# Optimization experiments

Hardware: AMD Instinct MI355X
Metric: run time of the kernel (lower is better)

## Reference

```python
import jax, jax.numpy as jnp
import numpy as np

B, L, D, M = 4, 8192, 512, 256
EPS = 1e-6


def _feature_map(x, proj, is_query):
    # FAVOR+ positive softmax-kernel features.
    # x: (B, L, D), proj: (M, D) with orthogonal rows scaled by sqrt(D).
    d = x.shape[-1]
    xs = x * (d ** -0.25)                      # scale by d^{-1/4}
    dash = jnp.einsum('bld,md->blm', xs, proj)  # (B, L, M)
    diag = 0.5 * jnp.sum(xs * xs, axis=-1, keepdims=True)  # (B, L, 1)
    if is_query:
        stab = jnp.max(dash, axis=-1, keepdims=True)        # per-position max
    else:
        stab = jnp.max(dash, axis=(-2, -1), keepdims=True)  # per-batch max
    return jnp.exp(dash - diag - stab) / jnp.sqrt(jnp.asarray(M, x.dtype)) + EPS


def setup_inputs() -> dict:
    key = jax.random.key(0)
    kq, kk, kv, kp = jax.random.split(key, 4)
    Q = jax.random.normal(kq, (B, L, D), dtype=jnp.float32)
    K = jax.random.normal(kk, (B, L, D), dtype=jnp.float32)
    V = jax.random.normal(kv, (B, L, D), dtype=jnp.float32)
    # Orthogonal random projection: QR of a Gaussian, rows scaled by sqrt(D).
    G = jax.random.normal(kp, (D, M), dtype=jnp.float32)
    q, _ = jnp.linalg.qr(G)                     # (D, M), orthonormal columns
    proj = q.T * jnp.sqrt(jnp.asarray(D, jnp.float32))  # (M, D)
    return {"Q": Q, "K": K, "V": V, "proj": proj}


def reference(Q, K, V, proj):
    Qf = _feature_map(Q, proj, is_query=True)   # (B, L, M)
    Kf = _feature_map(K, proj, is_query=False)  # (B, L, M)
    # Linear attention: aggregate keys/values once, O(L*M*D).
    KV = jnp.einsum('blm,bld->bmd', Kf, V)      # (B, M, D)
    Ksum = jnp.sum(Kf, axis=1)                  # (B, M)
    Z = 1.0 / (jnp.einsum('blm,bm->bl', Qf, Ksum) + EPS)  # (B, L)
    out = jnp.einsum('blm,bmd->bld', Qf, KV) * Z[..., None]
    return out
```

## Files before the change

kernel.cpp:

```cpp
#include <hip/hip_runtime.h>
#include <math.h>

typedef unsigned short u16;
typedef unsigned int u32;
typedef __attribute__((ext_vector_type(8))) short bf16x8;
typedef __attribute__((ext_vector_type(4))) float f32x4;

#define SCALE_ 0.21022410381342864f
#define EPS_ 1e-6f
#define RSQM_ 0.0625f
#define L_ 8192
#define PL_OFF_ 131072
#define KVL_OFF_ 524288

__device__ __forceinline__ float bf2f(u16 h) {
    return __uint_as_float(((u32)h) << 16);
}
__device__ __forceinline__ u32 cvtpk(float x0, float x1) {
    u32 w;
    asm("v_cvt_pk_bf16_f32 %0, %1, %2" : "=v"(w) : "v"(x0), "v"(x1));
    return w;
}
__device__ __forceinline__ void split_pk(float x0, float x1, u32& hw, u32& lw) {
    hw = cvtpk(x0, x1);
    float h0 = __uint_as_float(hw << 16);
    float h1 = __uint_as_float(hw & 0xffff0000u);
    lw = cvtpk(x0 - h0, x1 - h1);
}
__device__ __forceinline__ u32 okey(float x) {
    u32 b = __float_as_uint(x);
    return (b & 0x80000000u) ? ~b : (b | 0x80000000u);
}
__device__ __forceinline__ float odec(u32 k) {
    return (k & 0x80000000u) ? __uint_as_float(k & 0x7fffffffu) : __uint_as_float(~k);
}

#define GLDS16(gsrc, ldst) \
    __builtin_amdgcn_global_load_lds((__attribute__((address_space(1))) void*)(gsrc), \
                                     (__attribute__((address_space(3))) void*)(ldst), 16, 0, 0)

__global__ __launch_bounds__(256) void split_p(const float* __restrict__ P,
        u16* __restrict__ Ph, u16* __restrict__ Pl, u32* __restrict__ bmax) {
    if (blockIdx.x == 0 && threadIdx.x < 4) bmax[threadIdx.x] = 0u;
    int i = (blockIdx.x * 256 + threadIdx.x) * 2;
    u32 hw, lw;
    split_pk(P[i] * SCALE_, P[i + 1] * SCALE_, hw, lw);
    *reinterpret_cast<u32*>(&Ph[i]) = hw;
    *reinterpret_cast<u32*>(&Pl[i]) = lw;
}

__global__ __launch_bounds__(256) void dash_all(
        const float* __restrict__ Qg, const float* __restrict__ Kg,
        const u16* __restrict__ Bh_g,
        u16* __restrict__ QF, u16* __restrict__ KfT, float* __restrict__ ksump,
        u32* __restrict__ bmax) {
    __shared__ __align__(16) u16 Ah[64 * 32], Al[64 * 32];
    __shared__ __align__(16) u16 Bh[256 * 32], Bl[256 * 32];
    const int qpath = !(blockIdx.x & 1);
    const int tile = blockIdx.x >> 1;
    const float* __restrict__ X = qpath ? Qg : Kg;
    const int t = threadIdx.x, lane = t & 63;
    const int wid = t >> 6;
    const int row0 = tile * 64;
    const int l15 = lane & 15, l4 = lane >> 4;
    const int sr = t >> 2;
    const int awz = sr * 32 + (((t & 3) ^ ((sr >> 1) & 3)) * 8);
    const int koff = (l4 ^ ((l15 >> 1) & 3)) * 8;
    float ss = 0.f;

    const float* xp = &X[(size_t)(row0 + sr) * 512 + (t & 3) * 8];
    const u16* bsrch[4];
#pragma unroll
    for (int it = 0; it < 4; ++it) {
        const int m = it * 64 + wid * 16 + (lane >> 2);
        const int swz = ((lane & 3) ^ ((m >> 1) & 3)) * 8;
        bsrch[it] = Bh_g + (size_t)m * 512 + swz;
    }

    f32x4 acc[4][4];
#pragma unroll
    for (int i = 0; i < 4; ++i)
#pragma unroll
        for (int j = 0; j < 4; ++j) acc[i][j] = (f32x4){0.f, 0.f, 0.f, 0.f};

    float4 v0 = *reinterpret_cast<const float4*>(xp);
    float4 v1 = *reinterpret_cast<const float4*>(xp + 4);

    for (int kt = 0; kt < 16; ++kt) {
        __syncthreads();
        {
#pragma unroll
            for (int it = 0; it < 4; ++it) {
                GLDS16(bsrch[it], Bh + it * 2048 + wid * 512);
                GLDS16(bsrch[it] + PL_OFF_, Bl + it * 2048 + wid * 512);
                bsrch[it] += 32;
            }
            float xs[8] = {v0.x, v0.y, v0.z, v0.w, v1.x, v1.y, v1.z, v1.w};
#pragma unroll
            for (int i = 0; i < 8; ++i) ss = fmaf(xs[i], xs[i], ss);
            u32 hw[4], lw[4];
#pragma unroll
            for (int i = 0; i < 4; ++i) split_pk(xs[2 * i], xs[2 * i + 1], hw[i], lw[i]);
            *reinterpret_cast<uint4*>(&Ah[awz]) = make_uint4(hw[0], hw[1], hw[2], hw[3]);
            *reinterpret_cast<uint4*>(&Al[awz]) = make_uint4(lw[0], lw[1], lw[2], lw[3]);
            xp = (kt < 15) ? xp + 32 : xp;
            v0 = *reinterpret_cast<const float4*>(xp);
            v1 = *reinterpret_cast<const float4*>(xp + 4);
        }
        __syncthreads();
        bf16x8 a_h[4], a_l[4];
#pragma unroll
        for (int mf = 0; mf < 4; ++mf) {
            int r = (mf * 16 + l15) * 32 + koff;
            a_h[mf] = *reinterpret_cast<const bf16x8*>(&Ah[r]);
            a_l[mf] = *reinterpret_cast<const bf16x8*>(&Al[r]);
        }
#pragma unroll
        for (int nf = 0; nf < 4; ++nf) {
            const int r = (wid * 64 + nf * 16 + l15) * 32 + koff;
            bf16x8 b_h = *reinterpret_cast<const bf16x8*>(&Bh[r]);
            bf16x8 b_l = *reinterpret_cast<const bf16x8*>(&Bl[r]);
#pragma unroll
            for (int mf = 0; mf < 4; ++mf) {
                acc[mf][nf] = __builtin_amdgcn_mfma_f32_16x16x32_bf16(a_h[mf], b_h, acc[mf][nf], 0, 0, 0);
                acc[mf][nf] = __builtin_amdgcn_mfma_f32_16x16x32_bf16(a_h[mf], b_l, acc[mf][nf], 0, 0, 0);
                acc[mf][nf] = __builtin_amdgcn_mfma_f32_16x16x32_bf16(a_l[mf], b_h, acc[mf][nf], 0, 0, 0);
            }
        }
    }
    __syncthreads();
    float* rmaxp = reinterpret_cast<float*>(Ah);
    float* diagp = reinterpret_cast<float*>(Al);

    ss += __shfl_xor(ss, 1);
    ss += __shfl_xor(ss, 2);
    if ((t & 3) == 0) diagp[sr] = 0.5f * SCALE_ * SCALE_ * ss;

    if (qpath) {
        float rm[4][4];
#pragma unroll
        for (int mf = 0; mf < 4; ++mf)
#pragma unroll
            for (int r = 0; r < 4; ++r) {
                float v = fmaxf(fmaxf(acc[mf][0][r], acc[mf][1][r]),
                                fmaxf(acc[mf][2][r], acc[mf][3][r]));
#pragma unroll
                for (int off = 1; off < 16; off <<= 1) v = fmaxf(v, __shfl_xor(v, off));
                rm[mf][r] = v;
            }
        if (l15 == 0) {
#pragma unroll
            for (int mf = 0; mf < 4; ++mf)
#pragma unroll
                for (int r = 0; r < 4; ++r)
                    rmaxp[(mf * 16 + l4 * 4 + r) * 4 + wid] = rm[mf][r];
        }
        __syncthreads();
#pragma unroll
        for (int mf = 0; mf < 4; ++mf)
#pragma unroll
            for (int r = 0; r < 4; ++r) {
                const int rl = mf * 16 + l4 * 4 + r;
                float m4 = fmaxf(fmaxf(rmaxp[rl * 4 + 0], rmaxp[rl * 4 + 1]),
                                 fmaxf(rmaxp[rl * 4 + 2], rmaxp[rl * 4 + 3]));
                const float c = diagp[rl] + m4;
                float f0 = expf(acc[mf][0][r] - c) * RSQM_ + EPS_;
                float f1 = expf(acc[mf][1][r] - c) * RSQM_ + EPS_;
                float f2 = expf(acc[mf][2][r] - c) * RSQM_ + EPS_;
                float f3 = expf(acc[mf][3][r] - c) * RSQM_ + EPS_;
                u32 w01 = cvtpk(f0, f1), w23 = cvtpk(f2, f3);
                size_t o = (size_t)(row0 + rl) * 256 + wid * 64 + l15;
                QF[o]      = (u16)w01;
                QF[o + 16] = (u16)(w01 >> 16);
                QF[o + 32] = (u16)w23;
                QF[o + 48] = (u16)(w23 >> 16);
            }
    } else {
        __syncthreads();
        const int b = row0 >> 13;
        const int ll = row0 & 8191;
        float bm = -1e30f;
        float s[4] = {0.f, 0.f, 0.f, 0.f};
#pragma unroll
        for (int nf = 0; nf < 4; ++nf) {
            const size_t mb = ((size_t)(b * 256 + wid * 64 + nf * 16 + l15)) * 8192 + ll + l4 * 4;
#pragma unroll
            for (int mf = 0; mf < 4; ++mf) {
                float e0 = acc[mf][nf][0], e1 = acc[mf][nf][1];
                float e2 = acc[mf][nf][2], e3 = acc[mf][nf][3];
                bm = fmaxf(fmaxf(bm, fmaxf(e0, e1)), fmaxf(e2, e3));
                float x0 = expf(e0 - diagp[mf * 16 + l4 * 4 + 0]);
                float x1 = expf(e1 - diagp[mf * 16 + l4 * 4 + 1]);
                float x2 = expf(e2 - diagp[mf * 16 + l4 * 4 + 2]);
                float x3 = expf(e3 - diagp[mf * 16 + l4 * 4 + 3]);
                s[nf] += (x0 + x1) + (x2 + x3);
                uint2 w = make_uint2(cvtpk(x0, x1), cvtpk(x2, x3));
                *reinterpret_cast<uint2*>(&KfT[mb + mf * 16]) = w;
            }
        }
#pragma unroll
        for (int nf = 0; nf < 4; ++nf) {
            s[nf] += __shfl_xor(s[nf], 16);
            s[nf] += __shfl_xor(s[nf], 32);
        }
        if (l4 == 0) {
#pragma unroll
            for (int nf = 0; nf < 4; ++nf)
                ksump[tile * 256 + wid * 64 + nf * 16 + l15] = s[nf];
        }
#pragma unroll
        for (int off = 1; off < 64; off <<= 1) bm = fmaxf(bm, __shfl_xor(bm, off));
        if (lane == 0) diagp[64 + wid] = bm;
        __syncthreads();
        if (t == 0) {
            float m = fmaxf(fmaxf(diagp[64], diagp[65]), fmaxf(diagp[66], diagp[67]));
            atomicMax(&bmax[b], okey(m));
        }
    }
}

__global__ __launch_bounds__(256) void split_vt(const float* __restrict__ V,
        u16* __restrict__ Vt, float* __restrict__ vsump) {
    const int dt = blockIdx.x & 7, lt = blockIdx.x >> 3;
    const int lg = lt * 64, b = lg >> 13, d0 = dt * 64;
    __shared__ u16 T[64][72];
    const int t = threadIdx.x;
    const int lrow = t >> 2, c0 = (t & 3) * 16;
#pragma unroll
    for (int ii = 0; ii < 4; ++ii) {
        float4 v = *reinterpret_cast<const float4*>(&V[(size_t)(lg + lrow) * 512 + d0 + c0 + ii * 4]);
        *reinterpret_cast<u32*>(&T[lrow][c0 + ii * 4 + 0]) = cvtpk(v.x, v.y);
        *reinterpret_cast<u32*>(&T[lrow][c0 + ii * 4 + 2]) = cvtpk(v.z, v.w);
    }
    __syncthreads();
    const int dloc = t >> 2, lc = (t & 3) * 16;
    u32 w[8];
    float s = 0.f;
#pragma unroll
    for (int j = 0; j < 8; ++j) {
        u16 a = T[lc + 2 * j][dloc], c = T[lc + 2 * j + 1][dloc];
        w[j] = (u32)a | ((u32)c << 16);
        s += bf2f(a) + bf2f(c);
    }
    size_t ob = ((size_t)(b * 512 + d0 + dloc)) * 8192 + (lg & 8191) + lc;
    reinterpret_cast<uint4*>(&Vt[ob])[0] = make_uint4(w[0], w[1], w[2], w[3]);
    reinterpret_cast<uint4*>(&Vt[ob])[1] = make_uint4(w[4], w[5], w[6], w[7]);
    s += __shfl_xor(s, 1);
    s += __shfl_xor(s, 2);
    if ((t & 3) == 0) vsump[lt * 512 + d0 + dloc] = s;
}

__global__ __launch_bounds__(256) void ksum_red(const float* __restrict__ ksump,
        const u32* __restrict__ bmax, float* __restrict__ KsumT) {
    const int b = blockIdx.x, m = threadIdx.x;
    float s = 0.f;
    for (int j = 0; j < 128; ++j) s += ksump[(b * 128 + j) * 256 + m];
    const float g = expf(-odec(bmax[b]));
    KsumT[b * 256 + m] = g * s + (float)L_ * EPS_;
}

__global__ __launch_bounds__(256) void vsum_red(const float* __restrict__ vsump,
        float* __restrict__ Vsum) {
    const int idx = blockIdx.x * 256 + threadIdx.x;
    const int b = idx >> 9, d = idx & 511;
    float s = 0.f;
    for (int j = 0; j < 128; ++j) s += vsump[(b * 128 + j) * 512 + d];
    Vsum[idx] = s;
}

__global__ __launch_bounds__(256) void kv_mfma(
        const u16* __restrict__ KfT, const u16* __restrict__ Vt,
        float* __restrict__ kvp) {
    int o = (blockIdx.x & 7) * 64 + (blockIdx.x >> 3);
    const int dt = o & 3, mt = (o >> 2) & 1, ch = (o >> 3) & 15, b = o >> 7;
    const u16* Ag = KfT + ((size_t)(b * 256 + mt * 128)) * 8192 + ch * 512;
    const u16* Bg = Vt + ((size_t)(b * 512 + dt * 128)) * 8192 + ch * 512;
    __shared__ __align__(16) u16 A_[128 * 32], B_[128 * 32];
    const int t = threadIdx.x, lane = t & 63;
    const int wid = t >> 6, wr = wid >> 1, wc = wid & 1;
    const int l15 = lane & 15, l4 = lane >> 4;
    const int koff = (l4 ^ ((l15 >> 1) & 3)) * 8;
    const u16* asrc[2];
    const u16* bsrc[2];
#pragma unroll
    for (int it = 0; it < 2; ++it) {
        const int row = it * 64 + wid * 16 + (lane >> 2);
        const int swz = ((lane & 3) ^ ((row >> 1) & 3)) * 8;
        asrc[it] = Ag + (size_t)row * 8192 + swz;
        bsrc[it] = Bg + (size_t)row * 8192 + swz;
    }
    f32x4 acc[4][4];
#pragma unroll
    for (int i = 0; i < 4; ++i)
#pragma unroll
        for (int j = 0; j < 4; ++j) acc[i][j] = (f32x4){0.f, 0.f, 0.f, 0.f};

    for (int kt = 0; kt < 16; ++kt) {
        __syncthreads();
#pragma unroll
        for (int it = 0; it < 2; ++it) {
            GLDS16(asrc[it], A_ + it * 2048 + wid * 512);
            GLDS16(bsrc[it], B_ + it * 2048 + wid * 512);
            asrc[it] += 32; bsrc[it] += 32;
        }
        __syncthreads();
        bf16x8 a[4];
#pragma unroll
        for (int mf = 0; mf < 4; ++mf)
            a[mf] = *reinterpret_cast<const bf16x8*>(&A_[(wr * 64 + mf * 16 + l15) * 32 + koff]);
#pragma unroll
        for (int nf = 0; nf < 4; ++nf) {
            bf16x8 bb = *reinterpret_cast<const bf16x8*>(&B_[(wc * 64 + nf * 16 + l15) * 32 + koff]);
#pragma unroll
            for (int mf = 0; mf < 4; ++mf)
                acc[mf][nf] = __builtin_amdgcn_mfma_f32_16x16x32_bf16(a[mf], bb, acc[mf][nf], 0, 0, 0);
        }
    }
#pragma unroll
    for (int mf = 0; mf < 4; ++mf)
#pragma unroll
        for (int r = 0; r < 4; ++r) {
            size_t oo = ((size_t)(ch * 4 + b) * 256 + mt * 128 + wr * 64 + mf * 16 + l4 * 4 + r) * 512
                        + dt * 128 + wc * 64;
#pragma unroll
            for (int nf = 0; nf < 4; ++nf)
                kvp[oo + nf * 16 + l15] = acc[mf][nf][r];
        }
}

__global__ __launch_bounds__(256) void kv_fix(const float* __restrict__ kvp,
        const u32* __restrict__ bmax, const float* __restrict__ Vsum,
        u16* __restrict__ KVth, u16* __restrict__ KVtl) {
    const int dt = blockIdx.x & 7, mt = (blockIdx.x >> 3) & 3, b = blockIdx.x >> 5;
    const int m0 = mt * 64, d0 = dt * 64;
    __shared__ u16 Th[64][72], Tl[64][72];
    const int t = threadIdx.x, mloc = t >> 2, c0 = (t & 3) * 16;
    float s[16];
#pragma unroll
    for (int j = 0; j < 16; ++j) s[j] = 0.f;
    for (int c = 0; c < 16; ++c) {
        size_t base = ((size_t)(c * 4 + b) * 256 + m0 + mloc) * 512 + d0 + c0;
#pragma unroll
        for (int ii = 0; ii < 4; ++ii) {
            float4 v = *reinterpret_cast<const float4*>(&kvp[base + ii * 4]);
            s[ii * 4 + 0] += v.x; s[ii * 4 + 1] += v.y;
            s[ii * 4 + 2] += v.z; s[ii * 4 + 3] += v.w;
        }
    }
    const float g = expf(-odec(bmax[b]));
#pragma unroll
    for (int j = 0; j < 16; j += 2) {
        float v0 = g * s[j]     + EPS_ * Vsum[b * 512 + d0 + c0 + j];
        float v1 = g * s[j + 1] + EPS_ * Vsum[b * 512 + d0 + c0 + j + 1];
        u32 hw, lw; split_pk(v0, v1, hw, lw);
        *reinterpret_cast<u32*>(&Th[mloc][c0 + j]) = hw;
        *reinterpret_cast<u32*>(&Tl[mloc][c0 + j]) = lw;
    }
    __syncthreads();
    const int dloc = t >> 2, mc = (t & 3) * 16;
    size_t ob = ((size_t)(b * 512 + d0 + dloc)) * 256 + m0 + mc;
    u32 wh[8], wl[8];
#pragma unroll
    for (int j = 0; j < 8; ++j) {
        wh[j] = (u32)Th[mc + 2 * j][dloc] | ((u32)Th[mc + 2 * j + 1][dloc] << 16);
        wl[j] = (u32)Tl[mc + 2 * j][dloc] | ((u32)Tl[mc + 2 * j + 1][dloc] << 16);
    }
    reinterpret_cast<uint4*>(&KVth[ob])[0] = make_uint4(wh[0], wh[1], wh[2], wh[3]);
    reinterpret_cast<uint4*>(&KVth[ob])[1] = make_uint4(wh[4], wh[5], wh[6], wh[7]);
    reinterpret_cast<uint4*>(&KVtl[ob])[0] = make_uint4(wl[0], wl[1], wl[2], wl[3]);
    reinterpret_cast<uint4*>(&KVtl[ob])[1] = make_uint4(wl[4], wl[5], wl[6], wl[7]);
}

__global__ __launch_bounds__(256) void z_kernel(const u16* __restrict__ QF,
        const float* __restrict__ KsumT, float* __restrict__ Z) {
    const int wid = threadIdx.x >> 6, lane = threadIdx.x & 63;
    const int row = blockIdx.x * 4 + wid;
    const int b = row >> 13;
    uint2 u = *reinterpret_cast<const uint2*>(&QF[(size_t)row * 256 + lane * 4]);
    float4 ks = *reinterpret_cast<const float4*>(&KsumT[b * 256 + lane * 4]);
    float s = bf2f((u16)(u.x & 0xffff)) * ks.x + bf2f((u16)(u.x >> 16)) * ks.y +
              bf2f((u16)(u.y & 0xffff)) * ks.z + bf2f((u16)(u.y >> 16)) * ks.w;
#pragma unroll
    for (int off = 1; off < 64; off <<= 1) s += __shfl_xor(s, off);
    if (lane == 0) Z[row] = 1.f / (s + EPS_);
}

__global__ __launch_bounds__(256) void out_mfma(
        const u16* __restrict__ QF, const u16* __restrict__ KVth,
        const float* __restrict__ Z, float* __restrict__ out) {
    int o = (blockIdx.x & 7) * 128 + (blockIdx.x >> 3);
    const int dt = o & 3, rt = o >> 2;
    const int row0 = rt * 128, b = row0 >> 13;
    const u16* Ag = QF + (size_t)row0 * 256;
    const u16* Bh_g = KVth + ((size_t)(b * 512 + dt * 128)) * 256;
    __shared__ __align__(16) u16 A_[128 * 32], Bh_[128 * 32], Bl_[128 * 32];
    const int t = threadIdx.x, lane = t & 63;
    const int wid = t >> 6, wr = wid >> 1, wc = wid & 1;
    const int l15 = lane & 15, l4 = lane >> 4;
    const int koff = (l4 ^ ((l15 >> 1) & 3)) * 8;
    const u16* asrc[2];
    const u16* bhsrc[2];
#pragma unroll
    for (int it = 0; it < 2; ++it) {
        const int row = it * 64 + wid * 16 + (lane >> 2);
        const int swz = ((lane & 3) ^ ((row >> 1) & 3)) * 8;
        asrc[it]  = Ag + (size_t)row * 256 + swz;
        bhsrc[it] = Bh_g + (size_t)row * 256 + swz;
    }
    f32x4 acc[4][4];
#pragma unroll
    for (int i = 0; i < 4; ++i)
#pragma unroll
        for (int j = 0; j < 4; ++j) acc[i][j] = (f32x4){0.f, 0.f, 0.f, 0.f};

    for (int kt = 0; kt < 8; ++kt) {
        __syncthreads();
#pragma unroll
        for (int it = 0; it < 2; ++it) {
            GLDS16(asrc[it], A_ + it * 2048 + wid * 512);
            GLDS16(bhsrc[it], Bh_ + it * 2048 + wid * 512);
            GLDS16(bhsrc[it] + KVL_OFF_, Bl_ + it * 2048 + wid * 512);
            asrc[it] += 32; bhsrc[it] += 32;
        }
        __syncthreads();
        bf16x8 a[4];
#pragma unroll
        for (int mf = 0; mf < 4; ++mf)
            a[mf] = *reinterpret_cast<const bf16x8*>(&A_[(wr * 64 + mf * 16 + l15) * 32 + koff]);
#pragma unroll
        for (int nf = 0; nf < 4; ++nf) {
            const int r = (wc * 64 + nf * 16 + l15) * 32 + koff;
            bf16x8 bh = *reinterpret_cast<const bf16x8*>(&Bh_[r]);
            bf16x8 bl = *reinterpret_cast<const bf16x8*>(&Bl_[r]);
#pragma unroll
            for (int mf = 0; mf < 4; ++mf) {
                acc[mf][nf] = __builtin_amdgcn_mfma_f32_16x16x32_bf16(a[mf], bh, acc[mf][nf], 0, 0, 0);
                acc[mf][nf] = __builtin_amdgcn_mfma_f32_16x16x32_bf16(a[mf], bl, acc[mf][nf], 0, 0, 0);
            }
        }
    }
#pragma unroll
    for (int mf = 0; mf < 4; ++mf)
#pragma unroll
        for (int r = 0; r < 4; ++r) {
            const int row = row0 + wr * 64 + mf * 16 + l4 * 4 + r;
            const float z = Z[row];
#pragma unroll
            for (int nf = 0; nf < 4; ++nf)
                out[(size_t)row * 512 + dt * 128 + wc * 64 + nf * 16 + l15] = acc[mf][nf][r] * z;
        }
}

extern "C" void kernel_launch(void* const* d_in, const int* in_sizes, int n_in,
                              void* d_out, int out_size, void* d_ws, size_t ws_size,
                              hipStream_t stream) {
    const float* Q = (const float*)d_in[0];
    const float* K = (const float*)d_in[1];
    const float* V = (const float*)d_in[2];
    const float* P = (const float*)d_in[3];
    float* out = (float*)d_out;
    char* ws = (char*)d_ws;

    u16*   QF    = (u16*)(ws + 0);
    u16*   KfT   = (u16*)(ws + 16777216);
    u16*   Vt    = (u16*)(ws + 33554432);
    float* kvp   = (float*)(ws + 67108864);
    u16*   KVth  = (u16*)(ws + 100663296);
    u16*   KVtl  = (u16*)(ws + 101711872);
    u16*   PH    = (u16*)(ws + 102760448);
    u16*   PL    = (u16*)(ws + 103022592);
    float* ksump = (float*)(ws + 103284736);
    float* vsump = (float*)(ws + 103809024);
    float* KsumT = (float*)(ws + 104857600);
    float* Vsum  = (float*)(ws + 104861696);
    float* Zbuf  = (float*)(ws + 104869888);
    u32*   bmax  = (u32*)(ws + 105000960);

    split_p<<<256, 256, 0, stream>>>(P, PH, PL, bmax);
    dash_all<<<1024, 256, 0, stream>>>(Q, K, PH, QF, KfT, ksump, bmax);
    split_vt<<<4096, 256, 0, stream>>>(V, Vt, vsump);
    ksum_red<<<4, 256, 0, stream>>>(ksump, bmax, KsumT);
    vsum_red<<<8, 256, 0, stream>>>(vsump, Vsum);
    kv_mfma<<<512, 256, 0, stream>>>(KfT, Vt, kvp);
    kv_fix<<<128, 256, 0, stream>>>(kvp, bmax, Vsum, KVth, KVtl);
    z_kernel<<<8192, 256, 0, stream>>>(QF, KsumT, Zbuf);
    out_mfma<<<1024, 256, 0, stream>>>(QF, KVth, Zbuf, out);
}
```

Measured before the change: 173.8 us.

## Split dash_all tile across eight waves in a 2x4 grid

Doubles the dash_all block to 512 threads and arranges the waves as 2 row groups by 4 column groups, so each wave computes half as many row fragments. A-tile staging, B loads, the diag/max reductions and the ksump partial layout are reworked to match, and ksum_red now sums two partials per tile. The aim is more waves in flight per block to hide the latency of global and LDS loads. In exchange each B fragment is loaded from LDS by twice as many waves, and per-thread register use and occupancy change.

Result: slower. 191.8 us (+10.4%).

```diff
diff --git a/kernel.cpp b/kernel.cpp
--- a/kernel.cpp
+++ b/kernel.cpp
@@ -49,7 +49,7 @@
     *reinterpret_cast<u32*>(&Pl[i]) = lw;
 }
 
-__global__ __launch_bounds__(256) void dash_all(
+__global__ __launch_bounds__(512) void dash_all(
         const float* __restrict__ Qg, const float* __restrict__ Kg,
         const u16* __restrict__ Bh_g,
         u16* __restrict__ QF, u16* __restrict__ KfT, float* __restrict__ ksump,
@@ -61,67 +61,67 @@
     const float* __restrict__ X = qpath ? Qg : Kg;
     const int t = threadIdx.x, lane = t & 63;
     const int wid = t >> 6;
+    const int wr = wid >> 2, wc = wid & 3;
     const int row0 = tile * 64;
     const int l15 = lane & 15, l4 = lane >> 4;
-    const int sr = t >> 2;
-    const int awz = sr * 32 + (((t & 3) ^ ((sr >> 1) & 3)) * 8);
     const int koff = (l4 ^ ((l15 >> 1) & 3)) * 8;
+
+    const int sr = t >> 3;
+    const int ac = (t & 7) * 4;
+    const int awz = sr * 32 + ((((ac >> 3) ^ ((sr >> 1) & 3)) << 3) + (ac & 7));
     float ss = 0.f;
-
-    const float* xp = &X[(size_t)(row0 + sr) * 512 + (t & 3) * 8];
-    const u16* bsrch[4];
-#pragma unroll
-    for (int it = 0; it < 4; ++it) {
-        const int m = it * 64 + wid * 16 + (lane >> 2);
-        const int swz = ((lane & 3) ^ ((m >> 1) & 3)) * 8;
+    const float* xp = &X[(size_t)(row0 + sr) * 512 + ac];
+
+    const u16* bsrch[2];
+#pragma unroll
+    for (int it = 0; it < 2; ++it) {
+        const int m = it * 128 + (t >> 2);
+        const int swz = ((t & 3) ^ ((m >> 1) & 3)) * 8;
         bsrch[it] = Bh_g + (size_t)m * 512 + swz;
     }
 
-    f32x4 acc[4][4];
-#pragma unroll
-    for (int i = 0; i < 4; ++i)
+    f32x4 acc[2][4];
+#pragma unroll
+    for (int i = 0; i < 2; ++i)
 #pragma unroll
         for (int j = 0; j < 4; ++j) acc[i][j] = (f32x4){0.f, 0.f, 0.f, 0.f};
 
-    float4 v0 = *reinterpret_cast<const float4*>(xp);
-    float4 v1 = *reinterpret_cast<const float4*>(xp + 4);
+    float4 v = *reinterpret_cast<const float4*>(xp);
 
     for (int kt = 0; kt < 16; ++kt) {
         __syncthreads();
         {
 #pragma unroll
-            for (int it = 0; it < 4; ++it) {
-                GLDS16(bsrch[it], Bh + it * 2048 + wid * 512);
-                GLDS16(bsrch[it] + PL_OFF_, Bl + it * 2048 + wid * 512);
+            for (int it = 0; it < 2; ++it) {
+                GLDS16(bsrch[it], Bh + it * 4096 + wid * 512);
+                GLDS16(bsrch[it] + PL_OFF_, Bl + it * 4096 + wid * 512);
                 bsrch[it] += 32;
             }
-            float xs[8] = {v0.x, v0.y, v0.z, v0.w, v1.x, v1.y, v1.z, v1.w};
-#pragma unroll
-            for (int i = 0; i < 8; ++i) ss = fmaf(xs[i], xs[i], ss);
-            u32 hw[4], lw[4];
-#pragma unroll
-            for (int i = 0; i < 4; ++i) split_pk(xs[2 * i], xs[2 * i + 1], hw[i], lw[i]);
-            *reinterpret_cast<uint4*>(&Ah[awz]) = make_uint4(hw[0], hw[1], hw[2], hw[3]);
-            *reinterpret_cast<uint4*>(&Al[awz]) = make_uint4(lw[0], lw[1], lw[2], lw[3]);
+            ss = fmaf(v.x, v.x, ss); ss = fmaf(v.y, v.y, ss);
+            ss = fmaf(v.z, v.z, ss); ss = fmaf(v.w, v.w, ss);
+            u32 h0, l0, h1, l1;
+            split_pk(v.x, v.y, h0, l0);
+            split_pk(v.z, v.w, h1, l1);
+            *reinterpret_cast<uint2*>(&Ah[awz]) = make_uint2(h0, h1);
+            *reinterpret_cast<uint2*>(&Al[awz]) = make_uint2(l0, l1);
             xp = (kt < 15) ? xp + 32 : xp;
-            v0 = *reinterpret_cast<const float4*>(xp);
-            v1 = *reinterpret_cast<const float4*>(xp + 4);
-        }
-        __syncthreads();
-        bf16x8 a_h[4], a_l[4];
-#pragma unroll
-        for (int mf = 0; mf < 4; ++mf) {
-            int r = (mf * 16 + l15) * 32 + koff;
+            v = *reinterpret_cast<const float4*>(xp);
+        }
+        __syncthreads();
+        bf16x8 a_h[2], a_l[2];
+#pragma unroll
+        for (int mf = 0; mf < 2; ++mf) {
+            int r = (wr * 32 + mf * 16 + l15) * 32 + koff;
             a_h[mf] = *reinterpret_cast<const bf16x8*>(&Ah[r]);
             a_l[mf] = *reinterpret_cast<const bf16x8*>(&Al[r]);
         }
 #pragma unroll
         for (int nf = 0; nf < 4; ++nf) {
-            const int r = (wid * 64 + nf * 16 + l15) * 32 + koff;
+            const int r = (wc * 64 + nf * 16 + l15) * 32 + koff;
             bf16x8 b_h = *reinterpret_cast<const bf16x8*>(&Bh[r]);
             bf16x8 b_l = *reinterpret_cast<const bf16x8*>(&Bl[r]);
 #pragma unroll
-            for (int mf = 0; mf < 4; ++mf) {
+            for (int mf = 0; mf < 2; ++mf) {
                 acc[mf][nf] = __builtin_amdgcn_mfma_f32_16x16x32_bf16(a_h[mf], b_h, acc[mf][nf], 0, 0, 0);
                 acc[mf][nf] = __builtin_amdgcn_mfma_f32_16x16x32_bf16(a_h[mf], b_l, acc[mf][nf], 0, 0, 0);
                 acc[mf][nf] = __builtin_amdgcn_mfma_f32_16x16x32_bf16(a_l[mf], b_h, acc[mf][nf], 0, 0, 0);
@@ -134,33 +134,34 @@
 
     ss += __shfl_xor(ss, 1);
     ss += __shfl_xor(ss, 2);
-    if ((t & 3) == 0) diagp[sr] = 0.5f * SCALE_ * SCALE_ * ss;
+    ss += __shfl_xor(ss, 4);
+    if ((t & 7) == 0) diagp[sr] = 0.5f * SCALE_ * SCALE_ * ss;
 
     if (qpath) {
-        float rm[4][4];
-#pragma unroll
-        for (int mf = 0; mf < 4; ++mf)
+        float rm[2][4];
+#pragma unroll
+        for (int mf = 0; mf < 2; ++mf)
 #pragma unroll
             for (int r = 0; r < 4; ++r) {
-                float v = fmaxf(fmaxf(acc[mf][0][r], acc[mf][1][r]),
+                float x = fmaxf(fmaxf(acc[mf][0][r], acc[mf][1][r]),
                                 fmaxf(acc[mf][2][r], acc[mf][3][r]));
 #pragma unroll
-                for (int off = 1; off < 16; off <<= 1) v = fmaxf(v, __shfl_xor(v, off));
-                rm[mf][r] = v;
+                for (int off = 1; off < 16; off <<= 1) x = fmaxf(x, __shfl_xor(x, off));
+                rm[mf][r] = x;
             }
         if (l15 == 0) {
 #pragma unroll
-            for (int mf = 0; mf < 4; ++mf)
+            for (int mf = 0; mf < 2; ++mf)
 #pragma unroll
                 for (int r = 0; r < 4; ++r)
-                    rmaxp[(mf * 16 + l4 * 4 + r) * 4 + wid] = rm[mf][r];
-        }
-        __syncthreads();
-#pragma unroll
-        for (int mf = 0; mf < 4; ++mf)
+                    rmaxp[(wr * 32 + mf * 16 + l4 * 4 + r) * 4 + wc] = rm[mf][r];
+        }
+        __syncthreads();
+#pragma unroll
+        for (int mf = 0; mf < 2; ++mf)
 #pragma unroll
             for (int r = 0; r < 4; ++r) {
-                const int rl = mf * 16 + l4 * 4 + r;
+                const int rl = wr * 32 + mf * 16 + l4 * 4 + r;
                 float m4 = fmaxf(fmaxf(rmaxp[rl * 4 + 0], rmaxp[rl * 4 + 1]),
                                  fmaxf(rmaxp[rl * 4 + 2], rmaxp[rl * 4 + 3]));
                 const float c = diagp[rl] + m4;
@@ -169,7 +170,7 @@
                 float f2 = expf(acc[mf][2][r] - c) * RSQM_ + EPS_;
                 float f3 = expf(acc[mf][3][r] - c) * RSQM_ + EPS_;
                 u32 w01 = cvtpk(f0, f1), w23 = cvtpk(f2, f3);
-                size_t o = (size_t)(row0 + rl) * 256 + wid * 64 + l15;
+                size_t o = (size_t)(row0 + rl) * 256 + wc * 64 + l15;
                 QF[o]      = (u16)w01;
                 QF[o + 16] = (u16)(w01 >> 16);
                 QF[o + 32] = (u16)w23;
@@ -183,16 +184,18 @@
         float s[4] = {0.f, 0.f, 0.f, 0.f};
 #pragma unroll
         for (int nf = 0; nf < 4; ++nf) {
-            const size_t mb = ((size_t)(b * 256 + wid * 64 + nf * 16 + l15)) * 8192 + ll + l4 * 4;
-#pragma unroll
-            for (int mf = 0; mf < 4; ++mf) {
+            const size_t mb = ((size_t)(b * 256 + wc * 64 + nf * 16 + l15)) * 8192
+                              + ll + wr * 32 + l4 * 4;
+#pragma unroll
+            for (int mf = 0; mf < 2; ++mf) {
                 float e0 = acc[mf][nf][0], e1 = acc[mf][nf][1];
                 float e2 = acc[mf][nf][2], e3 = acc[mf][nf][3];
                 bm = fmaxf(fmaxf(bm, fmaxf(e0, e1)), fmaxf(e2, e3));
-                float x0 = expf(e0 - diagp[mf * 16 + l4 * 4 + 0]);
-                float x1 = expf(e1 - diagp[mf * 16 + l4 * 4 + 1]);
-                float x2 = expf(e2 - diagp[mf * 16 + l4 * 4 + 2]);
-                float x3 = expf(e3 - diagp[mf * 16 + l4 * 4 + 3]);
+                const int rb = wr * 32 + mf * 16 + l4 * 4;
+                float x0 = expf(e0 - diagp[rb + 0]);
+                float x1 = expf(e1 - diagp[rb + 1]);
+                float x2 = expf(e2 - diagp[rb + 2]);
+                float x3 = expf(e3 - diagp[rb + 3]);
                 s[nf] += (x0 + x1) + (x2 + x3);
                 uint2 w = make_uint2(cvtpk(x0, x1), cvtpk(x2, x3));
                 *reinterpret_cast<uint2*>(&KfT[mb + mf * 16]) = w;
@@ -206,14 +209,16 @@
         if (l4 == 0) {
 #pragma unroll
             for (int nf = 0; nf < 4; ++nf)
-                ksump[tile * 256 + wid * 64 + nf * 16 + l15] = s[nf];
+                ksump[(size_t)tile * 512 + wr * 256 + wc * 64 + nf * 16 + l15] = s[nf];
         }
 #pragma unroll
         for (int off = 1; off < 64; off <<= 1) bm = fmaxf(bm, __shfl_xor(bm, off));
         if (lane == 0) diagp[64 + wid] = bm;
         __syncthreads();
         if (t == 0) {
-            float m = fmaxf(fmaxf(diagp[64], diagp[65]), fmaxf(diagp[66], diagp[67]));
+            float m = diagp[64];
+#pragma unroll
+            for (int w2 = 1; w2 < 8; ++w2) m = fmaxf(m, diagp[64 + w2]);
             atomicMax(&bmax[b], okey(m));
         }
     }
@@ -254,7 +259,10 @@
         const u32* __restrict__ bmax, float* __restrict__ KsumT) {
     const int b = blockIdx.x, m = threadIdx.x;
     float s = 0.f;
-    for (int j = 0; j < 128; ++j) s += ksump[(b * 128 + j) * 256 + m];
+    for (int j = 0; j < 128; ++j) {
+        size_t base = (size_t)(b * 128 + j) * 512 + m;
+        s += ksump[base] + ksump[base + 256];
+    }
     const float g = expf(-odec(bmax[b]));
     KsumT[b * 256 + m] = g * s + (float)L_ * EPS_;
 }
@@ -470,14 +478,14 @@
     u16*   PH    = (u16*)(ws + 102760448);
     u16*   PL    = (u16*)(ws + 103022592);
     float* ksump = (float*)(ws + 103284736);
-    float* vsump = (float*)(ws + 103809024);
-    float* KsumT = (float*)(ws + 104857600);
-    float* Vsum  = (float*)(ws + 104861696);
-    float* Zbuf  = (float*)(ws + 104869888);
-    u32*   bmax  = (u32*)(ws + 105000960);
+    float* vsump = (float*)(ws + 104333312);
+    float* KsumT = (float*)(ws + 105381888);
+    float* Vsum  = (float*)(ws + 105385984);
+    float* Zbuf  = (float*)(ws + 105394176);
+    u32*   bmax  = (u32*)(ws + 105525248);
 
     split_p<<<256, 256, 0, stream>>>(P, PH, PL, bmax);
-    dash_all<<<1024, 256, 0, stream>>>(Q, K, PH, QF, KfT, ksump, bmax);
+    dash_all<<<1024, 512, 0, stream>>>(Q, K, PH, QF, KfT, ksump, bmax);
     split_vt<<<4096, 256, 0, stream>>>(V, Vt, vsump);
     ksum_red<<<4, 256, 0, stream>>>(ksump, bmax, KsumT);
     vsum_red<<<8, 256, 0, stream>>>(vsump, Vsum);
```
